# Kernel optimization log

Hardware: AMD Instinct MI355X
Metric: run time of the kernel (lower is better)

The kernel has to match this reference:

```python
import jax, jax.numpy as jnp
import numpy as np

INPUT = 256
HIDDEN = 1024
OUTPUT = 256
B, T = 64, 512


def setup_inputs() -> dict:
    key = jax.random.key(0)
    ks = jax.random.split(key, 7)
    s_ih = 1.0 / np.sqrt(INPUT)
    s_hh = 1.0 / np.sqrt(HIDDEN)
    return {
        "input_seq": jax.random.normal(ks[0], (B, T, INPUT), jnp.float32),
        "W_ih": jax.random.uniform(ks[1], (INPUT, 4 * HIDDEN), jnp.float32, -s_ih, s_ih),
        "W_hh": jax.random.uniform(ks[2], (HIDDEN, 4 * HIDDEN), jnp.float32, -s_hh, s_hh),
        "b_ih": jax.random.uniform(ks[3], (4 * HIDDEN,), jnp.float32, -s_hh, s_hh),
        "b_hh": jax.random.uniform(ks[4], (4 * HIDDEN,), jnp.float32, -s_hh, s_hh),
        "W_out": jax.random.uniform(ks[5], (HIDDEN, OUTPUT), jnp.float32, -s_hh, s_hh),
        "b_out": jax.random.uniform(ks[6], (OUTPUT,), jnp.float32, -s_hh, s_hh),
    }


def _lstm_last_hidden(x, W_ih, W_hh, b_ih, b_hh):
    Bsz = x.shape[0]
    H = W_hh.shape[0]
    # Precompute input-side gate projections for all timesteps: [T, B, 4H]
    x_t = jnp.einsum('bti,ih->tbh', x, W_ih) + b_ih + b_hh

    def step(carry, xg):
        h, c = carry
        gates = xg + h @ W_hh  # [B, 4H]
        i, f, g, o = jnp.split(gates, 4, axis=-1)
        i = jax.nn.sigmoid(i)
        f = jax.nn.sigmoid(f)
        g = jnp.tanh(g)
        o = jax.nn.sigmoid(o)
        c = f * c + i * g
        h = o * jnp.tanh(c)
        return (h, c), None

    h0 = jnp.zeros((Bsz, H), x.dtype)
    c0 = jnp.zeros((Bsz, H), x.dtype)
    (h_last, _), _ = jax.lax.scan(step, (h0, c0), x_t)
    return h_last


def reference(input_seq, W_ih, W_hh, b_ih, b_hh, W_out, b_out):
    h_last = _lstm_last_hidden(input_seq, W_ih, W_hh, b_ih, b_hh)  # [B, H]
    return h_last @ W_out + b_out  # [B, OUTPUT]
```

## Files before the change

kernel.cpp:

```cpp
#include <hip/hip_runtime.h>
#include <hip/hip_bf16.h>
#include <cstdint>

#define HIDDEN 1024
#define INPUT  256
#define BATCH  64
#define TSTEPS 512
#define NGCOL  4096
#define KTOT   1280
#define HBUFN  65536

typedef __attribute__((ext_vector_type(8))) short bf16x8;
typedef __attribute__((ext_vector_type(4))) float f32x4;
typedef unsigned long long u64;
typedef unsigned int u32;

__device__ inline short f2bs(float f) {
    union { __hip_bfloat16 h; short s; } u;
    u.h = __float2bfloat16(f);
    return u.s;
}
__device__ inline unsigned short f2bu(float f) {
    union { __hip_bfloat16 h; unsigned short s; } u;
    u.h = __float2bfloat16(f);
    return u.s;
}

__global__ __launch_bounds__(256) void build_wt(
    const float* __restrict__ Whh, const float* __restrict__ Wih,
    __hip_bfloat16* __restrict__ Wt)
{
    int t = blockIdx.x * 256 + threadIdx.x;
    int col = t & 4095;
    int k0  = (t >> 12) * 16;
    __hip_bfloat16 tmp[16];
    if (k0 < HIDDEN) {
        #pragma unroll
        for (int i = 0; i < 16; ++i)
            tmp[i] = __float2bfloat16(Whh[(size_t)(k0 + i) * NGCOL + col]);
    } else {
        #pragma unroll
        for (int i = 0; i < 16; ++i)
            tmp[i] = __float2bfloat16(Wih[(size_t)(k0 - HIDDEN + i) * NGCOL + col]);
    }
    #pragma unroll
    for (int i = 0; i < 16; ++i)
        Wt[(size_t)col * KTOT + k0 + i] = tmp[i];
}

__global__ __launch_bounds__(256) void init_state(
    const float* __restrict__ bih, const float* __restrict__ bhh,
    float* __restrict__ bias, u32* __restrict__ hbuf)
{
    int i = blockIdx.x * 256 + threadIdx.x;
    if (i < NGCOL) bias[i] = bih[i] + bhh[i];
    hbuf[i] = 0u;
}

__global__ __launch_bounds__(512, 2) void lstm_persist(
    const __hip_bfloat16* __restrict__ Wt,
    const float* __restrict__ x,
    u32* __restrict__ hbuf,
    float* __restrict__ hf,
    const float* __restrict__ bias)
{
    __shared__ float pbuf[8][1025];

    const int tid  = threadIdx.x;
    const int i    = blockIdx.x;
    const int cg   = (i & 7) * 8 + ((i >> 3) & 7);
    const int bg   = i >> 6;
    const int wave = tid >> 6;
    const int lane = tid & 63;
    const int l15  = lane & 15;
    const int l4   = lane >> 4;
    const int b0   = bg * 16;
    const int n0   = cg * 16;

    const __hip_bfloat16* wrow = Wt + (size_t)(n0 + l15) * KTOT;
    bf16x8 w[5][4];
    #pragma unroll
    for (int c5 = 0; c5 < 5; ++c5) {
        const int kk = (wave + c5 * 8) * 32 + l4 * 8;
        #pragma unroll
        for (int g = 0; g < 4; ++g)
            w[c5][g] = *(const bf16x8*)(wrow + (size_t)g * 1024 * KTOT + kk);
    }

    const int br = tid >> 4;
    const int hc = tid & 15;
    float creg = 0.f;
    float bi = 0.f, bfr = 0.f, bgg = 0.f, bo = 0.f;
    if (tid < 256) {
        bi  = bias[0 * 1024 + n0 + hc];
        bfr = bias[1 * 1024 + n0 + hc];
        bgg = bias[2 * 1024 + n0 + hc];
        bo  = bias[3 * 1024 + n0 + hc];
    }

    const int hoff = (b0 + l15) * HIDDEN + wave * 32 + l4 * 8;
    const float* xrow = x + ((size_t)(b0 + l15) * TSTEPS) * INPUT + wave * 32 + l4 * 8;

    const int jj  = lane & 7;
    const int rr  = (lane >> 3) & 3;
    const int pcg = 2 * wave + (jj & 1) + 16 * ((jj >> 1) & 3);
    const int sentoff = (b0 + 4 * rr + 3) * HIDDEN + pcg * 16 + ((lane >= 32) ? 7 : 15);

    for (int t = 0; t < TSTEPS; ++t) {
        const u32* hb = hbuf + (t & 1) * HBUFN;
        u32*       ho = hbuf + ((t + 1) & 1) * HBUFN;

        bf16x8 afx;
        {
            const float* xf = xrow + (size_t)t * INPUT;
            float4 pa = *(const float4*)(xf);
            float4 pb = *(const float4*)(xf + 4);
            afx[0] = f2bs(pa.x); afx[1] = f2bs(pa.y); afx[2] = f2bs(pa.z); afx[3] = f2bs(pa.w);
            afx[4] = f2bs(pb.x); afx[5] = f2bs(pb.y); afx[6] = f2bs(pb.z); afx[7] = f2bs(pb.w);
        }
        f32x4 a0 = {0.f, 0.f, 0.f, 0.f};
        f32x4 a1 = a0, a2 = a0, a3 = a0;
        a0 = __builtin_amdgcn_mfma_f32_16x16x32_bf16(afx, w[4][0], a0, 0, 0, 0);
        a1 = __builtin_amdgcn_mfma_f32_16x16x32_bf16(afx, w[4][1], a1, 0, 0, 0);
        a2 = __builtin_amdgcn_mfma_f32_16x16x32_bf16(afx, w[4][2], a2, 0, 0, 0);
        a3 = __builtin_amdgcn_mfma_f32_16x16x32_bf16(afx, w[4][3], a3, 0, 0, 0);

        {
            const u32 wantu = (u32)t << 16;
            for (;;) {
                u32 v = __hip_atomic_load(hb + sentoff, __ATOMIC_RELAXED,
                                          __HIP_MEMORY_SCOPE_AGENT);
                if (__all(((v ^ wantu) & 0xFFFF0000u) == 0)) break;
                __builtin_amdgcn_s_sleep(1);
            }
        }

        const u64 want  = ((u64)(u32)t << 16) | ((u64)(u32)t << 48);
        const u64 emask = 0xFFFF0000FFFF0000ull;
        u64 hq[4][4];
        {
            u64 bad = 0;
            #pragma unroll
            for (int c5 = 0; c5 < 4; ++c5) {
                const u64* hp = (const u64*)(hb + hoff + c5 * 256);
                #pragma unroll
                for (int q = 0; q < 4; ++q) {
                    hq[c5][q] = __hip_atomic_load(hp + q, __ATOMIC_RELAXED,
                                                  __HIP_MEMORY_SCOPE_AGENT);
                    bad |= (hq[c5][q] ^ want) & emask;
                }
            }
            while (!__all(bad == 0)) {
                __builtin_amdgcn_s_sleep(1);
                bad = 0;
                #pragma unroll
                for (int c5 = 0; c5 < 4; ++c5) {
                    const u64* hp = (const u64*)(hb + hoff + c5 * 256);
                    #pragma unroll
                    for (int q = 0; q < 4; ++q) {
                        hq[c5][q] = __hip_atomic_load(hp + q, __ATOMIC_RELAXED,
                                                      __HIP_MEMORY_SCOPE_AGENT);
                        bad |= (hq[c5][q] ^ want) & emask;
                    }
                }
            }
        }
        bf16x8 afh[4];
        #pragma unroll
        for (int c5 = 0; c5 < 4; ++c5) {
            union { u32 p[4]; bf16x8 v; } u;
            #pragma unroll
            for (int q = 0; q < 4; ++q) {
                const u64 d = hq[c5][q];
                u.p[q] = (u32)(d & 0xFFFFu) | ((u32)(d >> 32) << 16);
            }
            afh[c5] = u.v;
        }

        #pragma unroll
        for (int c5 = 0; c5 < 4; ++c5) {
            a0 = __builtin_amdgcn_mfma_f32_16x16x32_bf16(afh[c5], w[c5][0], a0, 0, 0, 0);
            a1 = __builtin_amdgcn_mfma_f32_16x16x32_bf16(afh[c5], w[c5][1], a1, 0, 0, 0);
            a2 = __builtin_amdgcn_mfma_f32_16x16x32_bf16(afh[c5], w[c5][2], a2, 0, 0, 0);
            a3 = __builtin_amdgcn_mfma_f32_16x16x32_bf16(afh[c5], w[c5][3], a3, 0, 0, 0);
        }

        float* pw = &pbuf[wave][0];
        #pragma unroll
        for (int r = 0; r < 4; ++r) {
            const int row = l4 * 4 + r;
            pw[(0 * 16 + row) * 16 + l15] = a0[r];
            pw[(1 * 16 + row) * 16 + l15] = a1[r];
            pw[(2 * 16 + row) * 16 + l15] = a2[r];
            pw[(3 * 16 + row) * 16 + l15] = a3[r];
        }
        __syncthreads();

        if (tid < 256) {
            float gi = bi, gf = bfr, gg = bgg, go = bo;
            #pragma unroll
            for (int w8 = 0; w8 < 8; ++w8) {
                const float* p = &pbuf[w8][0];
                gi += p[(0 * 16 + br) * 16 + hc];
                gf += p[(1 * 16 + br) * 16 + hc];
                gg += p[(2 * 16 + br) * 16 + hc];
                go += p[(3 * 16 + br) * 16 + hc];
            }
            const float i_ = 1.f / (1.f + __expf(-gi));
            const float f_ = 1.f / (1.f + __expf(-gf));
            const float g_ = tanhf(gg);
            const float o_ = 1.f / (1.f + __expf(-go));
            creg = f_ * creg + i_ * g_;
            const float h = o_ * tanhf(creg);
            if (t == TSTEPS - 1) {
                hf[(b0 + br) * HIDDEN + n0 + hc] = h;
            } else {
                const u32 val = ((u32)(t + 1) << 16) | (u32)f2bu(h);
                __hip_atomic_store(ho + (b0 + br) * HIDDEN + n0 + hc, val,
                                   __ATOMIC_RELAXED, __HIP_MEMORY_SCOPE_AGENT);
            }
        }
        if (t == TSTEPS - 1) break;
        __syncthreads();
    }
}

__global__ __launch_bounds__(256) void out_proj(
    const float* __restrict__ hf, const float* __restrict__ Wout,
    const float* __restrict__ bout, float* __restrict__ out)
{
    const int b  = blockIdx.x;
    const int oc = threadIdx.x;
    const float* hb = hf + (size_t)b * HIDDEN;
    float a0 = 0.f, a1 = 0.f, a2 = 0.f, a3 = 0.f;
    for (int k = 0; k < HIDDEN; k += 4) {
        a0 += hb[k + 0] * Wout[(size_t)(k + 0) * 256 + oc];
        a1 += hb[k + 1] * Wout[(size_t)(k + 1) * 256 + oc];
        a2 += hb[k + 2] * Wout[(size_t)(k + 2) * 256 + oc];
        a3 += hb[k + 3] * Wout[(size_t)(k + 3) * 256 + oc];
    }
    out[b * 256 + oc] = (a0 + a1) + (a2 + a3) + bout[oc];
}

extern "C" void kernel_launch(void* const* d_in, const int* in_sizes, int n_in,
                              void* d_out, int out_size, void* d_ws, size_t ws_size,
                              hipStream_t stream)
{
    const float* x    = (const float*)d_in[0];
    const float* Wih  = (const float*)d_in[1];
    const float* Whh  = (const float*)d_in[2];
    const float* bih  = (const float*)d_in[3];
    const float* bhh  = (const float*)d_in[4];
    const float* Wout = (const float*)d_in[5];
    const float* bout = (const float*)d_in[6];
    float* out = (float*)d_out;

    char* ws = (char*)d_ws;
    size_t off = 0;
    auto alloc = [&](size_t bytes) -> void* {
        void* p = ws + off;
        off = (off + bytes + 255) & ~(size_t)255;
        return p;
    };
    __hip_bfloat16* Wt = (__hip_bfloat16*)alloc((size_t)NGCOL * KTOT * 2);
    u32*   hbuf = (u32*)alloc((size_t)2 * HBUFN * 4);
    float* bias = (float*)alloc((size_t)NGCOL * 4);
    float* hf   = (float*)alloc((size_t)BATCH * HIDDEN * 4);

    build_wt<<<1280, 256, 0, stream>>>(Whh, Wih, Wt);
    init_state<<<512, 256, 0, stream>>>(bih, bhh, bias, hbuf);
    lstm_persist<<<256, 512, 0, stream>>>(Wt, x, hbuf, hf, bias);
    out_proj<<<64, 256, 0, stream>>>(hf, Wout, bout, out);
}
```

Measured before the change: 2.973 ms.

## Retile LSTM blocks to 8 batch rows by 32 hidden columns, stream weights

Each block now handles 8 batch rows and 32 hidden units (128 gate columns) instead of 16×16. Weights are no longer held in registers; they are reloaded from global memory/L2 every timestep. Half of each MFMA's A rows are zero padding, which wastes matrix throughput in exchange for fewer h rows each block has to poll. The extra sentinel poll is removed, and the LDS reduction buffer is reshaped to match the new tiling.

```diff
diff --git a/kernel.cpp b/kernel.cpp
--- a/kernel.cpp
+++ b/kernel.cpp
@@ -64,85 +64,74 @@
     float* __restrict__ hf,
     const float* __restrict__ bias)
 {
-    __shared__ float pbuf[8][1025];
+    __shared__ float pbuf[8][8][132];
 
     const int tid  = threadIdx.x;
     const int i    = blockIdx.x;
-    const int cg   = (i & 7) * 8 + ((i >> 3) & 7);
-    const int bg   = i >> 6;
+    const int k8   = i & 7;
+    const int m    = i >> 3;
+    const int bg   = m & 7;
+    const int cg   = k8 * 4 + (m >> 3);
     const int wave = tid >> 6;
     const int lane = tid & 63;
     const int l15  = lane & 15;
     const int l4   = lane >> 4;
-    const int b0   = bg * 16;
-    const int n0   = cg * 16;
-
-    const __hip_bfloat16* wrow = Wt + (size_t)(n0 + l15) * KTOT;
-    bf16x8 w[5][4];
+    const int b0   = bg * 8;
+    const int n0   = cg * 32;
+
+    const __hip_bfloat16* wcol[8];
     #pragma unroll
-    for (int c5 = 0; c5 < 5; ++c5) {
-        const int kk = (wave + c5 * 8) * 32 + l4 * 8;
-        #pragma unroll
-        for (int g = 0; g < 4; ++g)
-            w[c5][g] = *(const bf16x8*)(wrow + (size_t)g * 1024 * KTOT + kk);
-    }
-
-    const int br = tid >> 4;
-    const int hc = tid & 15;
+    for (int ct = 0; ct < 8; ++ct) {
+        const int tilecol = ct * 16 + l15;
+        const int g  = tilecol >> 5;
+        const int hc = tilecol & 31;
+        wcol[ct] = Wt + (size_t)(g * 1024 + n0 + hc) * KTOT;
+    }
+
+    const int rrow = tid >> 5;
+    const int rhc  = tid & 31;
     float creg = 0.f;
     float bi = 0.f, bfr = 0.f, bgg = 0.f, bo = 0.f;
     if (tid < 256) {
-        bi  = bias[0 * 1024 + n0 + hc];
-        bfr = bias[1 * 1024 + n0 + hc];
-        bgg = bias[2 * 1024 + n0 + hc];
-        bo  = bias[3 * 1024 + n0 + hc];
-    }
-
-    const int hoff = (b0 + l15) * HIDDEN + wave * 32 + l4 * 8;
-    const float* xrow = x + ((size_t)(b0 + l15) * TSTEPS) * INPUT + wave * 32 + l4 * 8;
-
-    const int jj  = lane & 7;
-    const int rr  = (lane >> 3) & 3;
-    const int pcg = 2 * wave + (jj & 1) + 16 * ((jj >> 1) & 3);
-    const int sentoff = (b0 + 4 * rr + 3) * HIDDEN + pcg * 16 + ((lane >= 32) ? 7 : 15);
+        bi  = bias[0 * 1024 + n0 + rhc];
+        bfr = bias[1 * 1024 + n0 + rhc];
+        bgg = bias[2 * 1024 + n0 + rhc];
+        bo  = bias[3 * 1024 + n0 + rhc];
+    }
+
+    const bool act = (l15 < 8);
+    const int  hrow = b0 + l15;
+    const float* xrow = x + ((size_t)hrow * TSTEPS) * INPUT + wave * 32 + l4 * 8;
+    const int  kkx = 1024 + wave * 32 + l4 * 8;
 
     for (int t = 0; t < TSTEPS; ++t) {
         const u32* hb = hbuf + (t & 1) * HBUFN;
         u32*       ho = hbuf + ((t + 1) & 1) * HBUFN;
 
-        bf16x8 afx;
-        {
+        bf16x8 afx = {0, 0, 0, 0, 0, 0, 0, 0};
+        if (act) {
             const float* xf = xrow + (size_t)t * INPUT;
             float4 pa = *(const float4*)(xf);
             float4 pb = *(const float4*)(xf + 4);
             afx[0] = f2bs(pa.x); afx[1] = f2bs(pa.y); afx[2] = f2bs(pa.z); afx[3] = f2bs(pa.w);
             afx[4] = f2bs(pb.x); afx[5] = f2bs(pb.y); afx[6] = f2bs(pb.z); afx[7] = f2bs(pb.w);
         }
-        f32x4 a0 = {0.f, 0.f, 0.f, 0.f};
-        f32x4 a1 = a0, a2 = a0, a3 = a0;
-        a0 = __builtin_amdgcn_mfma_f32_16x16x32_bf16(afx, w[4][0], a0, 0, 0, 0);
-        a1 = __builtin_amdgcn_mfma_f32_16x16x32_bf16(afx, w[4][1], a1, 0, 0, 0);
-        a2 = __builtin_amdgcn_mfma_f32_16x16x32_bf16(afx, w[4][2], a2, 0, 0, 0);
-        a3 = __builtin_amdgcn_mfma_f32_16x16x32_bf16(afx, w[4][3], a3, 0, 0, 0);
-
-        {
-            const u32 wantu = (u32)t << 16;
-            for (;;) {
-                u32 v = __hip_atomic_load(hb + sentoff, __ATOMIC_RELAXED,
-                                          __HIP_MEMORY_SCOPE_AGENT);
-                if (__all(((v ^ wantu) & 0xFFFF0000u) == 0)) break;
-                __builtin_amdgcn_s_sleep(1);
-            }
-        }
+        f32x4 acc[8];
+        #pragma unroll
+        for (int ct = 0; ct < 8; ++ct) acc[ct] = (f32x4){0.f, 0.f, 0.f, 0.f};
+        #pragma unroll
+        for (int ct = 0; ct < 8; ++ct)
+            acc[ct] = __builtin_amdgcn_mfma_f32_16x16x32_bf16(
+                afx, *(const bf16x8*)(wcol[ct] + kkx), acc[ct], 0, 0, 0);
 
         const u64 want  = ((u64)(u32)t << 16) | ((u64)(u32)t << 48);
         const u64 emask = 0xFFFF0000FFFF0000ull;
         u64 hq[4][4];
-        {
-            u64 bad = 0;
+        u64 bad = 0;
+        if (act) {
             #pragma unroll
             for (int c5 = 0; c5 < 4; ++c5) {
-                const u64* hp = (const u64*)(hb + hoff + c5 * 256);
+                const u64* hp = (const u64*)(hb + hrow * HIDDEN + (wave + c5 * 8) * 32 + l4 * 8);
                 #pragma unroll
                 for (int q = 0; q < 4; ++q) {
                     hq[c5][q] = __hip_atomic_load(hp + q, __ATOMIC_RELAXED,
@@ -150,12 +139,14 @@
                     bad |= (hq[c5][q] ^ want) & emask;
                 }
             }
-            while (!__all(bad == 0)) {
-                __builtin_amdgcn_s_sleep(1);
-                bad = 0;
+        }
+        while (!__all(bad == 0)) {
+            __builtin_amdgcn_s_sleep(1);
+            bad = 0;
+            if (act) {
                 #pragma unroll
                 for (int c5 = 0; c5 < 4; ++c5) {
-                    const u64* hp = (const u64*)(hb + hoff + c5 * 256);
+                    const u64* hp = (const u64*)(hb + hrow * HIDDEN + (wave + c5 * 8) * 32 + l4 * 8);
                     #pragma unroll
                     for (int q = 0; q < 4; ++q) {
                         hq[c5][q] = __hip_atomic_load(hp + q, __ATOMIC_RELAXED,
@@ -165,34 +156,34 @@
                 }
             }
         }
-        bf16x8 afh[4];
+
         #pragma unroll
         for (int c5 = 0; c5 < 4; ++c5) {
-            union { u32 p[4]; bf16x8 v; } u;
-            #pragma unroll
-            for (int q = 0; q < 4; ++q) {
-                const u64 d = hq[c5][q];
-                u.p[q] = (u32)(d & 0xFFFFu) | ((u32)(d >> 32) << 16);
-            }
-            afh[c5] = u.v;
-        }
-
-        #pragma unroll
-        for (int c5 = 0; c5 < 4; ++c5) {
-            a0 = __builtin_amdgcn_mfma_f32_16x16x32_bf16(afh[c5], w[c5][0], a0, 0, 0, 0);
-            a1 = __builtin_amdgcn_mfma_f32_16x16x32_bf16(afh[c5], w[c5][1], a1, 0, 0, 0);
-            a2 = __builtin_amdgcn_mfma_f32_16x16x32_bf16(afh[c5], w[c5][2], a2, 0, 0, 0);
-            a3 = __builtin_amdgcn_mfma_f32_16x16x32_bf16(afh[c5], w[c5][3], a3, 0, 0, 0);
-        }
-
-        float* pw = &pbuf[wave][0];
-        #pragma unroll
-        for (int r = 0; r < 4; ++r) {
-            const int row = l4 * 4 + r;
-            pw[(0 * 16 + row) * 16 + l15] = a0[r];
-            pw[(1 * 16 + row) * 16 + l15] = a1[r];
-            pw[(2 * 16 + row) * 16 + l15] = a2[r];
-            pw[(3 * 16 + row) * 16 + l15] = a3[r];
+            bf16x8 af = {0, 0, 0, 0, 0, 0, 0, 0};
+            if (act) {
+                union { u32 p[4]; bf16x8 v; } u;
+                #pragma unroll
+                for (int q = 0; q < 4; ++q) {
+                    const u64 d = hq[c5][q];
+                    u.p[q] = (u32)(d & 0xFFFFu) | ((u32)(d >> 32) << 16);
+                }
+                af = u.v;
+            }
+            const int kk = (wave + c5 * 8) * 32 + l4 * 8;
+            #pragma unroll
+            for (int ct = 0; ct < 8; ++ct)
+                acc[ct] = __builtin_amdgcn_mfma_f32_16x16x32_bf16(
+                    af, *(const bf16x8*)(wcol[ct] + kk), acc[ct], 0, 0, 0);
+        }
+
+        if (l4 < 2) {
+            #pragma unroll
+            for (int r = 0; r < 4; ++r) {
+                const int row = l4 * 4 + r;
+                #pragma unroll
+                for (int ct = 0; ct < 8; ++ct)
+                    pbuf[wave][row][ct * 16 + l15] = acc[ct][r];
+            }
         }
         __syncthreads();
 
@@ -200,11 +191,11 @@
             float gi = bi, gf = bfr, gg = bgg, go = bo;
             #pragma unroll
             for (int w8 = 0; w8 < 8; ++w8) {
-                const float* p = &pbuf[w8][0];
-                gi += p[(0 * 16 + br) * 16 + hc];
-                gf += p[(1 * 16 + br) * 16 + hc];
-                gg += p[(2 * 16 + br) * 16 + hc];
-                go += p[(3 * 16 + br) * 16 + hc];
+                const float* p = &pbuf[w8][rrow][0];
+                gi += p[0 * 32 + rhc];
+                gf += p[1 * 32 + rhc];
+                gg += p[2 * 32 + rhc];
+                go += p[3 * 32 + rhc];
             }
             const float i_ = 1.f / (1.f + __expf(-gi));
             const float f_ = 1.f / (1.f + __expf(-gf));
@@ -213,10 +204,10 @@
             creg = f_ * creg + i_ * g_;
             const float h = o_ * tanhf(creg);
             if (t == TSTEPS - 1) {
-                hf[(b0 + br) * HIDDEN + n0 + hc] = h;
+                hf[(b0 + rrow) * HIDDEN + n0 + rhc] = h;
             } else {
                 const u32 val = ((u32)(t + 1) << 16) | (u32)f2bu(h);
-                __hip_atomic_store(ho + (b0 + br) * HIDDEN + n0 + hc, val,
+                __hip_atomic_store(ho + (b0 + rrow) * HIDDEN + n0 + rhc, val,
                                    __ATOMIC_RELAXED, __HIP_MEMORY_SCOPE_AGENT);
             }
         }
```

Result: slower. 3.180 ms (+7.0%).
